# Performance work log

Measured on AMD Instinct MI355X. Metric: run time of the kernel, lower is better.

The kernel has to match this reference:

```python
import jax, jax.numpy as jnp
import numpy as np

LN_EPS = 1e-5

def setup_inputs() -> dict:
    key = jax.random.key(0)
    ks = jax.random.split(key, 4)
    B, T, D = 8, 2048, 1024
    x = jax.random.normal(ks[0], (B, T, D), dtype=jnp.float32)
    Wz = jax.random.normal(ks[1], (D, D), dtype=jnp.float32) * (1.0 / np.sqrt(D))
    bz = jnp.zeros((D,), dtype=jnp.float32)
    Wh = jax.random.normal(ks[2], (D, D), dtype=jnp.float32) * (1.0 / np.sqrt(D))
    bh = jnp.zeros((D,), dtype=jnp.float32)
    swish_beta = jnp.float32(1.0)
    ln_gamma = jnp.ones((D,), dtype=jnp.float32)
    ln_beta = jnp.zeros((D,), dtype=jnp.float32)
    return {"x": x, "Wz": Wz, "bz": bz, "Wh": Wh, "bh": bh,
            "swish_beta": swish_beta, "ln_gamma": ln_gamma, "ln_beta": ln_beta}

def _min_gru(x, Wz, bz, Wh, bh):
    # x: [B,T,D]. minGRU: h_t = (1-z_t)*h_{t-1} + z_t*h_tilde_t, h_0 = 0.
    z = jax.nn.sigmoid(jnp.einsum('btd,de->bte', x, Wz) + bz)   # [B,T,D]
    h_tilde = jnp.einsum('btd,de->bte', x, Wh) + bh             # [B,T,D]
    a = 1.0 - z
    b = z * h_tilde
    # parallel associative scan over time for h_t = a_t*h_{t-1} + b_t
    def combine(c1, c2):
        a1, b1 = c1
        a2, b2 = c2
        return a1 * a2, a2 * b1 + b2
    _, h = jax.lax.associative_scan(combine, (a, b), axis=1)
    return h  # [B,T,D]

def reference(x, Wz, bz, Wh, bh, swish_beta, ln_gamma, ln_beta):
    h = _min_gru(x, Wz, bz, Wh, bh)
    # Swish with learnable beta: silu(beta*x) = (beta*x)*sigmoid(beta*x)
    s = swish_beta * h
    y = s * jax.nn.sigmoid(s)
    # LayerNorm over last dim (channels_last)
    mu = jnp.mean(y, axis=-1, keepdims=True)
    var = jnp.mean(jnp.square(y - mu), axis=-1, keepdims=True)
    out = (y - mu) * jax.lax.rsqrt(var + LN_EPS) * ln_gamma + ln_beta
    return out
```

## Files before the change

kernel.cpp:

```cpp
#include <hip/hip_runtime.h>

#define GLOBAL_AS __attribute__((address_space(1)))
#define LDS_AS __attribute__((address_space(3)))

typedef unsigned short u16;
typedef unsigned int u32;
typedef __bf16 bf16x8 __attribute__((ext_vector_type(8)));
typedef float f32x4 __attribute__((ext_vector_type(4)));

static constexpr int BB = 8;
static constexpr int TT = 2048;
static constexpr int DD = 1024;
static constexpr int MM = BB * TT;
static constexpr int KK = DD;
static constexpr int NC = 64;
static constexpr int CL = TT / NC;
static constexpr int NCH = BB * NC;

__device__ __forceinline__ u16 f2bf(float f) {
  union { float f; u32 u; } c; c.f = f;
  u32 u = c.u;
  u32 r = (u + 0x7fffu + ((u >> 16) & 1u)) >> 16;
  return (u16)r;
}

__device__ __forceinline__ float bf2f(u16 b) {
  union { u32 u; float f; } c; c.u = ((u32)b) << 16;
  return c.f;
}

__global__ void cvt_x_kernel(const float* __restrict__ x, u16* __restrict__ xb) {
  int i = (blockIdx.x * blockDim.x + threadIdx.x) * 8;
  const float4* p = reinterpret_cast<const float4*>(x + i);
  float4 v0 = p[0], v1 = p[1];
  u16 r0 = f2bf(v0.x), r1 = f2bf(v0.y), r2 = f2bf(v0.z), r3 = f2bf(v0.w);
  u16 r4 = f2bf(v1.x), r5 = f2bf(v1.y), r6 = f2bf(v1.z), r7 = f2bf(v1.w);
  uint4 o;
  o.x = (u32)r0 | ((u32)r1 << 16);
  o.y = (u32)r2 | ((u32)r3 << 16);
  o.z = (u32)r4 | ((u32)r5 << 16);
  o.w = (u32)r6 | ((u32)r7 << 16);
  *reinterpret_cast<uint4*>(xb + i) = o;
}

__global__ void cvt_w_kernel(const float* __restrict__ Wz, const float* __restrict__ Wh,
                             u16* __restrict__ WT) {
  __shared__ float tile[32][33];
  int w = blockIdx.z;
  const float* W = w ? Wh : Wz;
  u16* O = WT + (size_t)w * DD * KK;
  int k0 = blockIdx.y * 32;
  int n0 = blockIdx.x * 32;
  int tx = threadIdx.x, ty = threadIdx.y;
  for (int i = 0; i < 32; i += 8)
    tile[ty + i][tx] = W[(size_t)(k0 + ty + i) * DD + n0 + tx];
  __syncthreads();
  for (int i = 0; i < 32; i += 8)
    O[(size_t)(n0 + ty + i) * KK + k0 + tx] = f2bf(tile[tx][ty + i]);
}

__global__ __launch_bounds__(256, 2) void gemm_dual_kernel(
    const u16* __restrict__ xb,
    const u16* __restrict__ WT,
    const float* __restrict__ bz, const float* __restrict__ bh,
    u32* __restrict__ ab_out,
    float* __restrict__ Asum, float* __restrict__ Bsum) {
  __shared__ __align__(16) u16 As[128 * 64];
  __shared__ __align__(16) u16 Bzs[128 * 64];
  __shared__ __align__(16) u16 Bhs[128 * 64];

  int bid = blockIdx.x;
  int swz = ((bid & 7) << 7) | (bid >> 3);
  int mt = swz >> 3;
  int nt = swz & 7;
  int m0 = mt * 128, n0 = nt * 128;

  int tid = threadIdx.x;
  int lane = tid & 63;
  int wave = tid >> 6;
  int wr = wave >> 1;
  int wc = wave & 1;

  int r0 = tid >> 3;
  int cswz = ((tid & 7) ^ ((tid >> 3) & 7)) << 3;
  const u16* Ag  = xb + (size_t)(m0 + r0) * KK + cswz;
  const u16* Bzg = WT + (size_t)(n0 + r0) * KK + cswz;
  const u16* Bhg = Bzg + (size_t)DD * KK;

  u16* AsW  = As  + wave * 512;
  u16* BzsW = Bzs + wave * 512;
  u16* BhsW = Bhs + wave * 512;

  f32x4 accz[4][4];
  f32x4 acch[4][4];
#pragma unroll
  for (int i = 0; i < 4; i++)
#pragma unroll
    for (int j = 0; j < 4; j++) {
      accz[i][j] = (f32x4){0.f, 0.f, 0.f, 0.f};
      acch[i][j] = (f32x4){0.f, 0.f, 0.f, 0.f};
    }

  int fr = lane & 15;
  int fk = (lane >> 4) * 8;
  const int swx = (fr & 7) << 3;

  for (int k0i = 0; k0i < KK; k0i += 64) {
#pragma unroll
    for (int q = 0; q < 4; q++) {
      __builtin_amdgcn_global_load_lds((const GLOBAL_AS void*)(Ag  + k0i + (size_t)(q * 32) * KK),
                                       (LDS_AS void*)(AsW + q * 2048), 16, 0, 0);
      __builtin_amdgcn_global_load_lds((const GLOBAL_AS void*)(Bzg + k0i + (size_t)(q * 32) * KK),
                                       (LDS_AS void*)(BzsW + q * 2048), 16, 0, 0);
      __builtin_amdgcn_global_load_lds((const GLOBAL_AS void*)(Bhg + k0i + (size_t)(q * 32) * KK),
                                       (LDS_AS void*)(BhsW + q * 2048), 16, 0, 0);
    }
    __syncthreads();

#pragma unroll
    for (int kk = 0; kk < 64; kk += 32) {
      bf16x8 af[4], bzf[4], bhf[4];
#pragma unroll
      for (int i = 0; i < 4; i++)
        af[i] = *reinterpret_cast<const bf16x8*>(
            As + (wr * 64 + i * 16 + fr) * 64 + ((kk + fk) ^ swx));
#pragma unroll
      for (int j = 0; j < 4; j++) {
        int br = wc * 64 + j * 16 + fr;
        bzf[j] = *reinterpret_cast<const bf16x8*>(Bzs + br * 64 + ((kk + fk) ^ swx));
        bhf[j] = *reinterpret_cast<const bf16x8*>(Bhs + br * 64 + ((kk + fk) ^ swx));
      }
#pragma unroll
      for (int i = 0; i < 4; i++)
#pragma unroll
        for (int j = 0; j < 4; j++) {
          accz[i][j] = __builtin_amdgcn_mfma_f32_16x16x32_bf16(af[i], bzf[j], accz[i][j], 0, 0, 0);
          acch[i][j] = __builtin_amdgcn_mfma_f32_16x16x32_bf16(af[i], bhf[j], acch[i][j], 0, 0, 0);
        }
    }
    __syncthreads();
  }

  int quad = lane >> 4;
#pragma unroll
  for (int j = 0; j < 4; j++) {
    int n = n0 + wc * 64 + j * 16 + fr;
    float bzv = bz[n], bhv = bh[n];
    float Ai[4], Bi[4];
#pragma unroll
    for (int i = 0; i < 4; i++) {
      float Aloc = 1.f, Bloc = 0.f;
      int mbase = m0 + wr * 64 + i * 16 + quad * 4;
#pragma unroll
      for (int r = 0; r < 4; r++) {
        float zp = accz[i][j][r] + bzv;
        float hp = acch[i][j][r] + bhv;
        float zs = 1.0f / (1.0f + __expf(-zp));
        float av = 1.0f - zs;
        float bv = zs * hp;
        u32 aq = (u32)(av * 65535.0f + 0.5f);
        if (aq > 65535u) aq = 65535u;
        u16 bb16 = f2bf(bv);
        size_t idx = (size_t)(mbase + r) * DD + n;
        ab_out[idx] = aq | ((u32)bb16 << 16);
        float avr = (float)aq * (1.0f / 65535.0f);
        float bvr = bf2f(bb16);
        Bloc = avr * Bloc + bvr;
        Aloc = avr * Aloc;
      }
      float Ao = __shfl_xor(Aloc, 16, 64);
      float Bo = __shfl_xor(Bloc, 16, 64);
      float Bc = (quad & 1) ? (Aloc * Bo + Bloc) : (Ao * Bloc + Bo);
      float Ac = Aloc * Ao;
      float Ao2 = __shfl_xor(Ac, 32, 64);
      float Bo2 = __shfl_xor(Bc, 32, 64);
      Bi[i] = (quad & 2) ? (Ac * Bo2 + Bc) : (Ao2 * Bc + Bo2);
      Ai[i] = Ac * Ao2;
    }
#pragma unroll
    for (int ic = 0; ic < 2; ic++) {
      float Ack = Ai[2 * ic + 1] * Ai[2 * ic];
      float Bck = Ai[2 * ic + 1] * Bi[2 * ic] + Bi[2 * ic + 1];
      if (quad == 0) {
        int cg = mt * 4 + wr * 2 + ic;
        Asum[(size_t)cg * DD + n] = Ack;
        Bsum[(size_t)cg * DD + n] = Bck;
      }
    }
  }
}

__global__ void chunk_scan_kernel(const float* __restrict__ Asum, const float* __restrict__ Bsum,
                                  float* __restrict__ hin) {
  int tid = blockIdx.x * blockDim.x + threadIdx.x;
  int d = tid & (DD - 1);
  int b = tid >> 10;
  float h = 0.f;
#pragma unroll
  for (int c = 0; c < NC; c++) {
    int i = (b * NC + c) * DD + d;
    hin[i] = h;
    h = Asum[i] * h + Bsum[i];
  }
}

__global__ __launch_bounds__(256) void apply_ln_kernel(
    const u32* __restrict__ ab, const float* __restrict__ hin,
    const float* __restrict__ sbeta, const float* __restrict__ gamma,
    const float* __restrict__ lbeta, float* __restrict__ out) {
  __shared__ float ps[2][4];
  __shared__ float pq[2][4];
  int ch = blockIdx.x;
  int wv = threadIdx.x >> 6;
  int lane = threadIdx.x & 63;
  int d = wv * 256 + lane * 4;
  int b = ch >> 6, c = ch & (NC - 1);
  float sb = sbeta[0];

  float4 g4 = *reinterpret_cast<const float4*>(gamma + d);
  float4 be4 = *reinterpret_cast<const float4*>(lbeta + d);
  float4 h4 = *reinterpret_cast<const float4*>(hin + (size_t)ch * DD + d);

  size_t base = ((size_t)b * TT + (size_t)c * CL) * DD + d;

  uint4 zR[3];
#pragma unroll
  for (int p = 0; p < 3; p++)
    zR[p] = *reinterpret_cast<const uint4*>(ab + base + (size_t)p * DD);

#pragma unroll
  for (int t = 0; t < CL; t++) {
    const int slot = t % 3;
    const int pslot = t & 1;
    uint4 pv = zR[slot];
    if (t + 3 < CL)
      zR[slot] = *reinterpret_cast<const uint4*>(ab + base + (size_t)(t + 3) * DD);
    {
      union { u32 u; float f; } cb;
      const float as = 1.0f / 65535.0f;
      float av;
      av = (float)(pv.x & 0xffffu) * as; cb.u = pv.x & 0xffff0000u;
      h4.x = av * h4.x + cb.f;
      av = (float)(pv.y & 0xffffu) * as; cb.u = pv.y & 0xffff0000u;
      h4.y = av * h4.y + cb.f;
      av = (float)(pv.z & 0xffffu) * as; cb.u = pv.z & 0xffff0000u;
      h4.z = av * h4.z + cb.f;
      av = (float)(pv.w & 0xffffu) * as; cb.u = pv.w & 0xffff0000u;
      h4.w = av * h4.w + cb.f;
    }
    float sx = sb * h4.x, sy = sb * h4.y, sz = sb * h4.z, sw = sb * h4.w;
    float4 y;
    y.x = sx / (1.0f + __expf(-sx));
    y.y = sy / (1.0f + __expf(-sy));
    y.z = sz / (1.0f + __expf(-sz));
    y.w = sw / (1.0f + __expf(-sw));
    float sum = y.x + y.y + y.z + y.w;
    float sq = y.x * y.x + y.y * y.y + y.z * y.z + y.w * y.w;
#pragma unroll
    for (int o = 32; o > 0; o >>= 1) {
      sum += __shfl_xor(sum, o, 64);
      sq += __shfl_xor(sq, o, 64);
    }
    if (lane == 0) { ps[pslot][wv] = sum; pq[pslot][wv] = sq; }
    __syncthreads();
    float tot = ps[pslot][0] + ps[pslot][1] + ps[pslot][2] + ps[pslot][3];
    float totq = pq[pslot][0] + pq[pslot][1] + pq[pslot][2] + pq[pslot][3];
    float mu = tot * (1.0f / DD);
    float var = totq * (1.0f / DD) - mu * mu;
    float inv = rsqrtf(fmaxf(var, 0.f) + 1e-5f);
    float4 o4;
    o4.x = (y.x - mu) * inv * g4.x + be4.x;
    o4.y = (y.y - mu) * inv * g4.y + be4.y;
    o4.z = (y.z - mu) * inv * g4.z + be4.z;
    o4.w = (y.w - mu) * inv * g4.w + be4.w;
    *reinterpret_cast<float4*>(out + base + (size_t)t * DD) = o4;
  }
}

extern "C" void kernel_launch(void* const* d_in, const int* in_sizes, int n_in,
                              void* d_out, int out_size, void* d_ws, size_t ws_size,
                              hipStream_t stream) {
  const float* x     = (const float*)d_in[0];
  const float* Wz    = (const float*)d_in[1];
  const float* bz    = (const float*)d_in[2];
  const float* Wh    = (const float*)d_in[3];
  const float* bh    = (const float*)d_in[4];
  const float* sbeta = (const float*)d_in[5];
  const float* gamma = (const float*)d_in[6];
  const float* lbeta = (const float*)d_in[7];
  float* out = (float*)d_out;

  char* ws = (char*)d_ws;
  u16* xb     = (u16*)ws;
  u16* WT     = (u16*)(ws + 33554432);
  u32* ab     = (u32*)(ws + 37748736);
  float* Asum = (float*)(ws + 104857600);
  float* Bsum = (float*)(ws + 106954752);
  float* hin  = (float*)(ws + 109051904);

  cvt_x_kernel<<<8192, 256, 0, stream>>>(x, xb);
  dim3 tw(32, 8), gw(32, 32, 2);
  cvt_w_kernel<<<gw, tw, 0, stream>>>(Wz, Wh, WT);
  gemm_dual_kernel<<<1024, 256, 0, stream>>>(xb, WT, bz, bh, ab, Asum, Bsum);
  chunk_scan_kernel<<<32, 256, 0, stream>>>(Asum, Bsum, hin);
  apply_ln_kernel<<<NCH, 256, 0, stream>>>(ab, hin, sbeta, gamma, lbeta, out);
}
```

Measured before the change: 234.0 us.

## Fuse conversion kernels and fold chunk-carry scan into apply kernel

```diff
diff --git a/kernel.cpp b/kernel.cpp
--- a/kernel.cpp
+++ b/kernel.cpp
@@ -29,34 +29,38 @@
   return c.f;
 }
 
-__global__ void cvt_x_kernel(const float* __restrict__ x, u16* __restrict__ xb) {
-  int i = (blockIdx.x * blockDim.x + threadIdx.x) * 8;
-  const float4* p = reinterpret_cast<const float4*>(x + i);
-  float4 v0 = p[0], v1 = p[1];
-  u16 r0 = f2bf(v0.x), r1 = f2bf(v0.y), r2 = f2bf(v0.z), r3 = f2bf(v0.w);
-  u16 r4 = f2bf(v1.x), r5 = f2bf(v1.y), r6 = f2bf(v1.z), r7 = f2bf(v1.w);
-  uint4 o;
-  o.x = (u32)r0 | ((u32)r1 << 16);
-  o.y = (u32)r2 | ((u32)r3 << 16);
-  o.z = (u32)r4 | ((u32)r5 << 16);
-  o.w = (u32)r6 | ((u32)r7 << 16);
-  *reinterpret_cast<uint4*>(xb + i) = o;
-}
-
-__global__ void cvt_w_kernel(const float* __restrict__ Wz, const float* __restrict__ Wh,
-                             u16* __restrict__ WT) {
-  __shared__ float tile[32][33];
-  int w = blockIdx.z;
-  const float* W = w ? Wh : Wz;
-  u16* O = WT + (size_t)w * DD * KK;
-  int k0 = blockIdx.y * 32;
-  int n0 = blockIdx.x * 32;
-  int tx = threadIdx.x, ty = threadIdx.y;
-  for (int i = 0; i < 32; i += 8)
-    tile[ty + i][tx] = W[(size_t)(k0 + ty + i) * DD + n0 + tx];
-  __syncthreads();
-  for (int i = 0; i < 32; i += 8)
-    O[(size_t)(n0 + ty + i) * KK + k0 + tx] = f2bf(tile[tx][ty + i]);
+__global__ __launch_bounds__(256) void cvt_fused_kernel(
+    const float* __restrict__ x, u16* __restrict__ xb,
+    const float* __restrict__ Wz, const float* __restrict__ Wh,
+    u16* __restrict__ WT) {
+  int bid = blockIdx.x;
+  int tid = threadIdx.x;
+  if (bid < 8192) {
+    int i = (bid * 256 + tid) * 8;
+    const float4* p = reinterpret_cast<const float4*>(x + i);
+    float4 v0 = p[0], v1 = p[1];
+    uint4 o;
+    o.x = (u32)f2bf(v0.x) | ((u32)f2bf(v0.y) << 16);
+    o.y = (u32)f2bf(v0.z) | ((u32)f2bf(v0.w) << 16);
+    o.z = (u32)f2bf(v1.x) | ((u32)f2bf(v1.y) << 16);
+    o.w = (u32)f2bf(v1.z) | ((u32)f2bf(v1.w) << 16);
+    *reinterpret_cast<uint4*>(xb + i) = o;
+  } else {
+    __shared__ float tile[32][33];
+    int wid = bid - 8192;
+    int w = wid >> 10;
+    int r = wid & 1023;
+    int n0 = (r & 31) * 32;
+    int k0 = (r >> 5) * 32;
+    const float* W = w ? Wh : Wz;
+    u16* O = WT + (size_t)w * DD * KK;
+    int tx = tid & 31, ty = tid >> 5;
+    for (int i = 0; i < 32; i += 8)
+      tile[ty + i][tx] = W[(size_t)(k0 + ty + i) * DD + n0 + tx];
+    __syncthreads();
+    for (int i = 0; i < 32; i += 8)
+      O[(size_t)(n0 + ty + i) * KK + k0 + tx] = f2bf(tile[tx][ty + i]);
+  }
 }
 
 __global__ __launch_bounds__(256, 2) void gemm_dual_kernel(
@@ -190,22 +194,9 @@
   }
 }
 
-__global__ void chunk_scan_kernel(const float* __restrict__ Asum, const float* __restrict__ Bsum,
-                                  float* __restrict__ hin) {
-  int tid = blockIdx.x * blockDim.x + threadIdx.x;
-  int d = tid & (DD - 1);
-  int b = tid >> 10;
-  float h = 0.f;
-#pragma unroll
-  for (int c = 0; c < NC; c++) {
-    int i = (b * NC + c) * DD + d;
-    hin[i] = h;
-    h = Asum[i] * h + Bsum[i];
-  }
-}
-
 __global__ __launch_bounds__(256) void apply_ln_kernel(
-    const u32* __restrict__ ab, const float* __restrict__ hin,
+    const u32* __restrict__ ab,
+    const float* __restrict__ Asum, const float* __restrict__ Bsum,
     const float* __restrict__ sbeta, const float* __restrict__ gamma,
     const float* __restrict__ lbeta, float* __restrict__ out) {
   __shared__ float ps[2][4];
@@ -219,7 +210,20 @@
 
   float4 g4 = *reinterpret_cast<const float4*>(gamma + d);
   float4 be4 = *reinterpret_cast<const float4*>(lbeta + d);
-  float4 h4 = *reinterpret_cast<const float4*>(hin + (size_t)ch * DD + d);
+
+  float4 h4 = {0.f, 0.f, 0.f, 0.f};
+  {
+    size_t srow = ((size_t)b * NC) * DD + d;
+#pragma unroll 4
+    for (int cc = 0; cc < c; cc++) {
+      float4 av = *reinterpret_cast<const float4*>(Asum + srow + (size_t)cc * DD);
+      float4 bv = *reinterpret_cast<const float4*>(Bsum + srow + (size_t)cc * DD);
+      h4.x = av.x * h4.x + bv.x;
+      h4.y = av.y * h4.y + bv.y;
+      h4.z = av.z * h4.z + bv.z;
+      h4.w = av.w * h4.w + bv.w;
+    }
+  }
 
   size_t base = ((size_t)b * TT + (size_t)c * CL) * DD + d;
 
@@ -296,12 +300,8 @@
   u32* ab     = (u32*)(ws + 37748736);
   float* Asum = (float*)(ws + 104857600);
   float* Bsum = (float*)(ws + 106954752);
-  float* hin  = (float*)(ws + 109051904);
-
-  cvt_x_kernel<<<8192, 256, 0, stream>>>(x, xb);
-  dim3 tw(32, 8), gw(32, 32, 2);
-  cvt_w_kernel<<<gw, tw, 0, stream>>>(Wz, Wh, WT);
+
+  cvt_fused_kernel<<<10240, 256, 0, stream>>>(x, xb, Wz, Wh, WT);
   gemm_dual_kernel<<<1024, 256, 0, stream>>>(xb, WT, bz, bh, ab, Asum, Bsum);
-  chunk_scan_kernel<<<32, 256, 0, stream>>>(Asum, Bsum, hin);
-  apply_ln_kernel<<<NCH, 256, 0, stream>>>(ab, hin, sbeta, gamma, lbeta, out);
-}
+  apply_ln_kernel<<<NCH, 256, 0, stream>>>(ab, Asum, Bsum, sbeta, gamma, lbeta, out);
+}
```

Measured after the change: 236.6 us. Within noise of the previous version (+1.1%).

## Double-buffer GEMM LDS tiles with K=32 stages to overlap loads and MFMA

Applied to the files above, without the earlier changes.

```diff
diff --git a/kernel.cpp b/kernel.cpp
--- a/kernel.cpp
+++ b/kernel.cpp
@@ -33,13 +33,11 @@
   int i = (blockIdx.x * blockDim.x + threadIdx.x) * 8;
   const float4* p = reinterpret_cast<const float4*>(x + i);
   float4 v0 = p[0], v1 = p[1];
-  u16 r0 = f2bf(v0.x), r1 = f2bf(v0.y), r2 = f2bf(v0.z), r3 = f2bf(v0.w);
-  u16 r4 = f2bf(v1.x), r5 = f2bf(v1.y), r6 = f2bf(v1.z), r7 = f2bf(v1.w);
   uint4 o;
-  o.x = (u32)r0 | ((u32)r1 << 16);
-  o.y = (u32)r2 | ((u32)r3 << 16);
-  o.z = (u32)r4 | ((u32)r5 << 16);
-  o.w = (u32)r6 | ((u32)r7 << 16);
+  o.x = (u32)f2bf(v0.x) | ((u32)f2bf(v0.y) << 16);
+  o.y = (u32)f2bf(v0.z) | ((u32)f2bf(v0.w) << 16);
+  o.z = (u32)f2bf(v1.x) | ((u32)f2bf(v1.y) << 16);
+  o.w = (u32)f2bf(v1.z) | ((u32)f2bf(v1.w) << 16);
   *reinterpret_cast<uint4*>(xb + i) = o;
 }
 
@@ -65,9 +63,9 @@
     const float* __restrict__ bz, const float* __restrict__ bh,
     u32* __restrict__ ab_out,
     float* __restrict__ Asum, float* __restrict__ Bsum) {
-  __shared__ __align__(16) u16 As[128 * 64];
-  __shared__ __align__(16) u16 Bzs[128 * 64];
-  __shared__ __align__(16) u16 Bhs[128 * 64];
+  __shared__ __align__(16) u16 As[2][128 * 32];
+  __shared__ __align__(16) u16 Bzs[2][128 * 32];
+  __shared__ __align__(16) u16 Bhs[2][128 * 32];
 
   int bid = blockIdx.x;
   int swz = ((bid & 7) << 7) | (bid >> 3);
@@ -81,15 +79,13 @@
   int wr = wave >> 1;
   int wc = wave & 1;
 
-  int r0 = tid >> 3;
-  int cswz = ((tid & 7) ^ ((tid >> 3) & 7)) << 3;
+  int r0 = tid >> 2;
+  int cswz = (((tid & 3) ^ ((tid >> 2) & 3)) << 3);
   const u16* Ag  = xb + (size_t)(m0 + r0) * KK + cswz;
   const u16* Bzg = WT + (size_t)(n0 + r0) * KK + cswz;
   const u16* Bhg = Bzg + (size_t)DD * KK;
 
-  u16* AsW  = As  + wave * 512;
-  u16* BzsW = Bzs + wave * 512;
-  u16* BhsW = Bhs + wave * 512;
+  int wofs = wave * 512;
 
   f32x4 accz[4][4];
   f32x4 acch[4][4];
@@ -103,43 +99,55 @@
 
   int fr = lane & 15;
   int fk = (lane >> 4) * 8;
-  const int swx = (fr & 7) << 3;
-
-  for (int k0i = 0; k0i < KK; k0i += 64) {
-#pragma unroll
-    for (int q = 0; q < 4; q++) {
-      __builtin_amdgcn_global_load_lds((const GLOBAL_AS void*)(Ag  + k0i + (size_t)(q * 32) * KK),
-                                       (LDS_AS void*)(AsW + q * 2048), 16, 0, 0);
-      __builtin_amdgcn_global_load_lds((const GLOBAL_AS void*)(Bzg + k0i + (size_t)(q * 32) * KK),
-                                       (LDS_AS void*)(BzsW + q * 2048), 16, 0, 0);
-      __builtin_amdgcn_global_load_lds((const GLOBAL_AS void*)(Bhg + k0i + (size_t)(q * 32) * KK),
-                                       (LDS_AS void*)(BhsW + q * 2048), 16, 0, 0);
-    }
+  const int kc = fk ^ ((fr & 3) << 3);
+
+#define STAGE(bf, ko)                                                                     \
+  {                                                                                       \
+    _Pragma("unroll")                                                                     \
+    for (int q = 0; q < 2; q++) {                                                         \
+      __builtin_amdgcn_global_load_lds((const GLOBAL_AS void*)(Ag + (ko) + (size_t)(q * 64) * KK),  \
+                                       (LDS_AS void*)(&As[bf][wofs + q * 2048]), 16, 0, 0);         \
+      __builtin_amdgcn_global_load_lds((const GLOBAL_AS void*)(Bzg + (ko) + (size_t)(q * 64) * KK), \
+                                       (LDS_AS void*)(&Bzs[bf][wofs + q * 2048]), 16, 0, 0);        \
+      __builtin_amdgcn_global_load_lds((const GLOBAL_AS void*)(Bhg + (ko) + (size_t)(q * 64) * KK), \
+                                       (LDS_AS void*)(&Bhs[bf][wofs + q * 2048]), 16, 0, 0);        \
+    }                                                                                     \
+  }
+
+#define COMPUTE(bf)                                                                       \
+  {                                                                                       \
+    bf16x8 af[4], bzf[4], bhf[4];                                                         \
+    _Pragma("unroll")                                                                     \
+    for (int i = 0; i < 4; i++)                                                           \
+      af[i] = *reinterpret_cast<const bf16x8*>(&As[bf][(wr * 64 + i * 16 + fr) * 32 + kc]); \
+    _Pragma("unroll")                                                                     \
+    for (int j = 0; j < 4; j++) {                                                         \
+      int br = (wc * 64 + j * 16 + fr) * 32 + kc;                                         \
+      bzf[j] = *reinterpret_cast<const bf16x8*>(&Bzs[bf][br]);                            \
+      bhf[j] = *reinterpret_cast<const bf16x8*>(&Bhs[bf][br]);                            \
+    }                                                                                     \
+    _Pragma("unroll")                                                                     \
+    for (int i = 0; i < 4; i++)                                                           \
+      _Pragma("unroll")                                                                   \
+      for (int j = 0; j < 4; j++) {                                                       \
+        accz[i][j] = __builtin_amdgcn_mfma_f32_16x16x32_bf16(af[i], bzf[j], accz[i][j], 0, 0, 0); \
+        acch[i][j] = __builtin_amdgcn_mfma_f32_16x16x32_bf16(af[i], bhf[j], acch[i][j], 0, 0, 0); \
+      }                                                                                   \
+  }
+
+  STAGE(0, 0);
+  __syncthreads();
+
+  for (int k = 0; k < KK; k += 64) {
+    STAGE(1, k + 32);
+    COMPUTE(0);
     __syncthreads();
-
-#pragma unroll
-    for (int kk = 0; kk < 64; kk += 32) {
-      bf16x8 af[4], bzf[4], bhf[4];
-#pragma unroll
-      for (int i = 0; i < 4; i++)
-        af[i] = *reinterpret_cast<const bf16x8*>(
-            As + (wr * 64 + i * 16 + fr) * 64 + ((kk + fk) ^ swx));
-#pragma unroll
-      for (int j = 0; j < 4; j++) {
-        int br = wc * 64 + j * 16 + fr;
-        bzf[j] = *reinterpret_cast<const bf16x8*>(Bzs + br * 64 + ((kk + fk) ^ swx));
-        bhf[j] = *reinterpret_cast<const bf16x8*>(Bhs + br * 64 + ((kk + fk) ^ swx));
-      }
-#pragma unroll
-      for (int i = 0; i < 4; i++)
-#pragma unroll
-        for (int j = 0; j < 4; j++) {
-          accz[i][j] = __builtin_amdgcn_mfma_f32_16x16x32_bf16(af[i], bzf[j], accz[i][j], 0, 0, 0);
-          acch[i][j] = __builtin_amdgcn_mfma_f32_16x16x32_bf16(af[i], bhf[j], acch[i][j], 0, 0, 0);
-        }
-    }
+    if (k + 64 < KK) STAGE(0, k + 64);
+    COMPUTE(1);
     __syncthreads();
   }
+#undef STAGE
+#undef COMPUTE
 
   int quad = lane >> 4;
 #pragma unroll
```

After: 249.6 us. +6.7%, slower.

## Halve scan chunk length, vectorize chunk scan, alias gate buffer into output

Applied to the files above, without the earlier changes.

```diff
diff --git a/kernel.cpp b/kernel.cpp
--- a/kernel.cpp
+++ b/kernel.cpp
@@ -13,7 +13,7 @@
 static constexpr int DD = 1024;
 static constexpr int MM = BB * TT;
 static constexpr int KK = DD;
-static constexpr int NC = 64;
+static constexpr int NC = 128;
 static constexpr int CL = TT / NC;
 static constexpr int NCH = BB * NC;
 
@@ -33,13 +33,11 @@
   int i = (blockIdx.x * blockDim.x + threadIdx.x) * 8;
   const float4* p = reinterpret_cast<const float4*>(x + i);
   float4 v0 = p[0], v1 = p[1];
-  u16 r0 = f2bf(v0.x), r1 = f2bf(v0.y), r2 = f2bf(v0.z), r3 = f2bf(v0.w);
-  u16 r4 = f2bf(v1.x), r5 = f2bf(v1.y), r6 = f2bf(v1.z), r7 = f2bf(v1.w);
   uint4 o;
-  o.x = (u32)r0 | ((u32)r1 << 16);
-  o.y = (u32)r2 | ((u32)r3 << 16);
-  o.z = (u32)r4 | ((u32)r5 << 16);
-  o.w = (u32)r6 | ((u32)r7 << 16);
+  o.x = (u32)f2bf(v0.x) | ((u32)f2bf(v0.y) << 16);
+  o.y = (u32)f2bf(v0.z) | ((u32)f2bf(v0.w) << 16);
+  o.z = (u32)f2bf(v1.x) | ((u32)f2bf(v1.y) << 16);
+  o.w = (u32)f2bf(v1.z) | ((u32)f2bf(v1.w) << 16);
   *reinterpret_cast<uint4*>(xb + i) = o;
 }
 
@@ -146,7 +144,6 @@
   for (int j = 0; j < 4; j++) {
     int n = n0 + wc * 64 + j * 16 + fr;
     float bzv = bz[n], bhv = bh[n];
-    float Ai[4], Bi[4];
 #pragma unroll
     for (int i = 0; i < 4; i++) {
       float Aloc = 1.f, Bloc = 0.f;
@@ -174,15 +171,10 @@
       float Ac = Aloc * Ao;
       float Ao2 = __shfl_xor(Ac, 32, 64);
       float Bo2 = __shfl_xor(Bc, 32, 64);
-      Bi[i] = (quad & 2) ? (Ac * Bo2 + Bc) : (Ao2 * Bc + Bo2);
-      Ai[i] = Ac * Ao2;
-    }
-#pragma unroll
-    for (int ic = 0; ic < 2; ic++) {
-      float Ack = Ai[2 * ic + 1] * Ai[2 * ic];
-      float Bck = Ai[2 * ic + 1] * Bi[2 * ic] + Bi[2 * ic + 1];
+      float Bck = (quad & 2) ? (Ac * Bo2 + Bc) : (Ao2 * Bc + Bo2);
+      float Ack = Ac * Ao2;
       if (quad == 0) {
-        int cg = mt * 4 + wr * 2 + ic;
+        int cg = mt * 8 + wr * 4 + i;
         Asum[(size_t)cg * DD + n] = Ack;
         Bsum[(size_t)cg * DD + n] = Bck;
       }
@@ -190,17 +182,23 @@
   }
 }
 
-__global__ void chunk_scan_kernel(const float* __restrict__ Asum, const float* __restrict__ Bsum,
-                                  float* __restrict__ hin) {
-  int tid = blockIdx.x * blockDim.x + threadIdx.x;
-  int d = tid & (DD - 1);
-  int b = tid >> 10;
-  float h = 0.f;
-#pragma unroll
+__global__ __launch_bounds__(64) void chunk_scan_kernel(
+    const float* __restrict__ Asum, const float* __restrict__ Bsum,
+    float* __restrict__ hin) {
+  int tid = blockIdx.x * 64 + threadIdx.x;
+  int d4 = (tid & 255) * 4;
+  int b = tid >> 8;
+  float4 h = {0.f, 0.f, 0.f, 0.f};
+#pragma unroll 4
   for (int c = 0; c < NC; c++) {
-    int i = (b * NC + c) * DD + d;
-    hin[i] = h;
-    h = Asum[i] * h + Bsum[i];
+    size_t i = ((size_t)(b * NC + c)) * DD + d4;
+    *reinterpret_cast<float4*>(hin + i) = h;
+    float4 av = *reinterpret_cast<const float4*>(Asum + i);
+    float4 bv = *reinterpret_cast<const float4*>(Bsum + i);
+    h.x = av.x * h.x + bv.x;
+    h.y = av.y * h.y + bv.y;
+    h.z = av.z * h.z + bv.z;
+    h.w = av.w * h.w + bv.w;
   }
 }
 
@@ -214,7 +212,7 @@
   int wv = threadIdx.x >> 6;
   int lane = threadIdx.x & 63;
   int d = wv * 256 + lane * 4;
-  int b = ch >> 6, c = ch & (NC - 1);
+  int b = ch >> 7, c = ch & (NC - 1);
   float sb = sbeta[0];
 
   float4 g4 = *reinterpret_cast<const float4*>(gamma + d);
@@ -293,15 +291,15 @@
   char* ws = (char*)d_ws;
   u16* xb     = (u16*)ws;
   u16* WT     = (u16*)(ws + 33554432);
-  u32* ab     = (u32*)(ws + 37748736);
-  float* Asum = (float*)(ws + 104857600);
-  float* Bsum = (float*)(ws + 106954752);
-  float* hin  = (float*)(ws + 109051904);
+  float* Asum = (float*)(ws + 37748736);
+  float* Bsum = (float*)(ws + 41943040);
+  float* hin  = (float*)(ws + 33554432);
+  u32* ab     = (u32*)out;
 
   cvt_x_kernel<<<8192, 256, 0, stream>>>(x, xb);
   dim3 tw(32, 8), gw(32, 32, 2);
   cvt_w_kernel<<<gw, tw, 0, stream>>>(Wz, Wh, WT);
   gemm_dual_kernel<<<1024, 256, 0, stream>>>(xb, WT, bz, bh, ab, Asum, Bsum);
-  chunk_scan_kernel<<<32, 256, 0, stream>>>(Asum, Bsum, hin);
+  chunk_scan_kernel<<<32, 64, 0, stream>>>(Asum, Bsum, hin);
   apply_ln_kernel<<<NCH, 256, 0, stream>>>(ab, hin, sbeta, gamma, lbeta, out);
 }
```

After: 235.3 us. About the same (+0.6%).
